# Kernel tuning notes

Measured on AMD Instinct MI355X. Metric: run time of the kernel, lower is better.

Reference implementation:

```python
import jax, jax.numpy as jnp
import numpy as np
import math

B, TSRC, TTGT, DM, DI, H = 2, 2048, 2048, 1024, 1024, 16
DH = DI // H
LN_EPS = 1e-5


def setup_inputs() -> dict:
    key = jax.random.key(0)
    ks = iter(jax.random.split(key, 40))
    def p(*shape):
        return jax.random.normal(next(ks), shape, jnp.float32) * 0.02
    inp = {
        "enc_out_vecs": jax.random.normal(next(ks), (B, TSRC, DM), jnp.float32),
        "output_vecs": jax.random.normal(next(ks), (B, TTGT, DM), jnp.float32),
    }
    for tag in ("dd", "ed"):
        inp["Wq_" + tag] = p(DM, DI); inp["bq_" + tag] = jnp.zeros((DI,), jnp.float32)
        inp["Wk_" + tag] = p(DM, DI); inp["bk_" + tag] = jnp.zeros((DI,), jnp.float32)
        inp["Wv_" + tag] = p(DM, DI); inp["bv_" + tag] = jnp.zeros((DI,), jnp.float32)
        inp["Wo_" + tag] = p(DI, DM); inp["bo_" + tag] = jnp.zeros((DM,), jnp.float32)
        inp["W1_" + tag] = p(DM, 2 * DM); inp["b1_" + tag] = jnp.zeros((2 * DM,), jnp.float32)
        inp["W2_" + tag] = p(2 * DM, DM); inp["b2_" + tag] = jnp.zeros((DM,), jnp.float32)
        inp["g1_" + tag] = jnp.ones((DM,), jnp.float32); inp["be1_" + tag] = jnp.zeros((DM,), jnp.float32)
        inp["g2_" + tag] = jnp.ones((DM,), jnp.float32); inp["be2_" + tag] = jnp.zeros((DM,), jnp.float32)
    return inp


def _ln(x, g, b):
    m = jnp.mean(x, axis=-1, keepdims=True)
    v = jnp.var(x, axis=-1, keepdims=True)
    return (x - m) * jax.lax.rsqrt(v + LN_EPS) * g + b


def _mha(xq, xkv, Wq, bq, Wk, bk, Wv, bv, causal):
    Bb, Tq, _ = xq.shape
    Tk = xkv.shape[1]
    q = (xq @ Wq + bq).reshape(Bb, Tq, H, DH)
    k = (xkv @ Wk + bk).reshape(Bb, Tk, H, DH)
    v = (xkv @ Wv + bv).reshape(Bb, Tk, H, DH)
    s = jnp.einsum("bqhd,bkhd->bhqk", q, k) / math.sqrt(DH)
    if causal:
        mask = jnp.where(jnp.arange(Tk)[None, :] > jnp.arange(Tq)[:, None], -jnp.inf, 0.0)
        s = s + mask
    w = jax.nn.softmax(s, axis=-1)
    return jnp.einsum("bhqk,bkhd->bqhd", w, v).reshape(Bb, Tq, H * DH)


def reference(enc_out_vecs, output_vecs,
              Wq_dd, bq_dd, Wk_dd, bk_dd, Wv_dd, bv_dd, Wo_dd, bo_dd,
              W1_dd, b1_dd, W2_dd, b2_dd, g1_dd, be1_dd, g2_dd, be2_dd,
              Wq_ed, bq_ed, Wk_ed, bk_ed, Wv_ed, bv_ed, Wo_ed, bo_ed,
              W1_ed, b1_ed, W2_ed, b2_ed, g1_ed, be1_ed, g2_ed, be2_ed):
    # masked self-attention over decoder inputs
    x = output_vecs
    a = _mha(x, x, Wq_dd, bq_dd, Wk_dd, bk_dd, Wv_dd, bv_dd, causal=True)
    x = _ln(a @ Wo_dd + bo_dd + x, g1_dd, be1_dd)
    x = _ln(x + jax.nn.relu(x @ W1_dd + b1_dd) @ W2_dd + b2_dd, g2_dd, be2_dd)
    # cross attention against encoder outputs
    a = _mha(x, enc_out_vecs, Wq_ed, bq_ed, Wk_ed, bk_ed, Wv_ed, bv_ed, causal=False)
    x = _ln(a @ Wo_ed + bo_ed + x, g1_ed, be1_ed)
    x = _ln(jax.nn.relu(x @ W1_ed + b1_ed) @ W2_ed + b2_ed + x, g2_ed, be2_ed)
    return x
```

## Files before the change

### kernel.cpp

```cpp
#include <hip/hip_runtime.h>
#include <stdint.h>

#define DEV __device__ __forceinline__
typedef unsigned short u16;
typedef __attribute__((ext_vector_type(8))) short bf16x8;
typedef __attribute__((ext_vector_type(4))) float f32x4;

#define AS1 __attribute__((address_space(1)))
#define AS3 __attribute__((address_space(3)))
#define WAITVM0 asm volatile("s_waitcnt vmcnt(0)" ::: "memory")
#define QSCALE 0.18033688011112042f

DEV u16 f2bf(float f) {
  union { float f; uint32_t u; } x; x.f = f;
  uint32_t r = x.u + 0x7fffu + ((x.u >> 16) & 1u);
  return (u16)(r >> 16);
}

DEV uint32_t cvt_pk_bf16(float a, float b) {
  uint32_t r;
  asm("v_cvt_pk_bf16_f32 %0, %1, %2" : "=v"(r) : "v"(a), "v"(b));
  return r;
}

__global__ __launch_bounds__(256) void k_cvt2(const float* __restrict__ a, const float* __restrict__ bsrc,
                                              u16* __restrict__ oa, u16* __restrict__ ob, int n4) {
  int i = blockIdx.x * blockDim.x + threadIdx.x;
  const float* s;
  u16* o;
  int k;
  if (i < n4) { s = a; o = oa; k = i; }
  else        { s = bsrc; o = ob; k = i - n4; }
  float4 v = reinterpret_cast<const float4*>(s)[k];
  reinterpret_cast<ushort4*>(o)[k] = make_ushort4(f2bf(v.x), f2bf(v.y), f2bf(v.z), f2bf(v.w));
}

struct WTJob { const float* W; u16* WT; int K, M, msh, start; };
struct WTJobs { WTJob j[12]; };

__global__ void k_wT_all(WTJobs jobs) {
  __shared__ float tile[32][33];
  int b = blockIdx.x;
  int i = 0;
#pragma unroll
  for (int t = 1; t < 12; ++t)
    if (b >= jobs.j[t].start) i = t;
  const WTJob J = jobs.j[i];
  int rel = b - J.start;
  int m0 = (rel & ((1 << J.msh) - 1)) << 5;
  int k0 = (rel >> J.msh) << 5;
  int tx = threadIdx.x, ty = threadIdx.y;
#pragma unroll
  for (int q = 0; q < 4; ++q)
    tile[ty + q * 8][tx] = J.W[(size_t)(k0 + ty + q * 8) * J.M + m0 + tx];
  __syncthreads();
#pragma unroll
  for (int q = 0; q < 4; ++q)
    J.WT[(size_t)(m0 + ty + q * 8) * J.K + k0 + tx] = f2bf(tile[tx][ty + q * 8]);
}

template<int R>
DEV void stage_tile(const u16* __restrict__ g, int strideElems, u16* lds, int tid, int wv) {
#pragma unroll
  for (int t = 0; t < R / 32; ++t) {
    int idx = t * 256 + tid;
    int row = idx >> 3;
    int b = (idx & 7) << 4;
    int sb = b ^ ((row & 7) << 4);
    const char* src = (const char*)g + (size_t)row * strideElems * 2 + sb;
    char* dst = (char*)lds + (size_t)(t * 256 + wv * 64) * 16;
    __builtin_amdgcn_global_load_lds((const AS1 void*)src, (AS3 void*)dst, 16, 0, 0);
  }
}

DEV bf16x8 lds_frag(const u16* lds, int row, int kel) {
  int off = row * 128 + ((kel * 2) ^ ((row & 7) << 4));
  return *(const bf16x8*)((const char*)lds + off);
}

template<int JT, int MODE>
__global__ __launch_bounds__(256) void k_gemm(const u16* __restrict__ A, int lda,
                                              const u16* __restrict__ BT,
                                              const float* __restrict__ bias,
                                              void* __restrict__ C, int ldc, int K) {
  constexpr int BN = JT * 32;
  __shared__ __align__(16) u16 A_lds[2][128 * 64];
  __shared__ __align__(16) u16 B_lds[2][BN * 64];
  const int tid = threadIdx.x, lane = tid & 63, wv = tid >> 6;
  const int wm = wv >> 1, wn = wv & 1;
  const int nwg = gridDim.x * gridDim.y;
  const int flat = blockIdx.y * gridDim.x + blockIdx.x;
  const int sw = (flat & 7) * (nwg >> 3) + (flat >> 3);
  const int bx = sw % gridDim.x, by = sw / gridDim.x;
  const int bm0 = by * 128, bn0 = bx * BN;
  const int lr = lane & 15, lk = (lane >> 4) * 8, r0 = (lane >> 4) * 4;

  f32x4 acc[4][JT];
#pragma unroll
  for (int i = 0; i < 4; ++i)
#pragma unroll
    for (int j = 0; j < JT; ++j) acc[i][j] = f32x4{0.f, 0.f, 0.f, 0.f};

  stage_tile<128>(A + (size_t)bm0 * lda, lda, A_lds[0], tid, wv);
  stage_tile<BN>(BT + (size_t)bn0 * K, K, B_lds[0], tid, wv);
  WAITVM0;
  __builtin_amdgcn_s_barrier();

  int cur = 0;
  for (int k0 = 0; k0 < K; k0 += 64) {
    if (k0 + 64 < K) {
      stage_tile<128>(A + (size_t)bm0 * lda + k0 + 64, lda, A_lds[cur ^ 1], tid, wv);
      stage_tile<BN>(BT + (size_t)bn0 * K + k0 + 64, K, B_lds[cur ^ 1], tid, wv);
    }
#pragma unroll
    for (int kk = 0; kk < 2; ++kk) {
      bf16x8 af[4], bfr[JT];
#pragma unroll
      for (int i = 0; i < 4; ++i) af[i] = lds_frag(A_lds[cur], wm * 64 + i * 16 + lr, kk * 32 + lk);
#pragma unroll
      for (int j = 0; j < JT; ++j) bfr[j] = lds_frag(B_lds[cur], wn * (JT * 16) + j * 16 + lr, kk * 32 + lk);
#pragma unroll
      for (int i = 0; i < 4; ++i)
#pragma unroll
        for (int j = 0; j < JT; ++j)
          acc[i][j] = __builtin_amdgcn_mfma_f32_16x16x32_bf16(af[i], bfr[j], acc[i][j], 0, 0, 0);
    }
    WAITVM0;
    __builtin_amdgcn_s_barrier();
    cur ^= 1;
  }

#pragma unroll
  for (int j = 0; j < JT; ++j) {
    int col = bn0 + wn * (JT * 16) + j * 16 + lr;
    float bv = bias[col];
#pragma unroll
    for (int i = 0; i < 4; ++i) {
      int rowb = bm0 + wm * 64 + i * 16 + r0;
      if constexpr (MODE == 0) {
#pragma unroll
        for (int r = 0; r < 4; ++r)
          ((float*)C)[(size_t)(rowb + r) * ldc + col] = acc[i][j][r] + bv;
      } else {
#pragma unroll
        for (int r = 0; r < 4; ++r) {
          float v = fmaxf(acc[i][j][r] + bv, 0.f);
          ((u16*)C)[(size_t)(rowb + r) * ldc + col] = f2bf(v);
        }
      }
    }
  }
}

__global__ __launch_bounds__(256) void k_qkv(const u16* __restrict__ Aq, const u16* __restrict__ Akv,
                                             const u16* __restrict__ BT,
                                             const float* __restrict__ bq, const float* __restrict__ bk,
                                             const float* __restrict__ bv,
                                             u16* __restrict__ Qb, u16* __restrict__ Kb,
                                             u16* __restrict__ Vt, int K) {
  __shared__ __align__(16) u16 A_lds[2][128 * 64];
  __shared__ __align__(16) u16 B_lds[2][128 * 64];
  const int tid = threadIdx.x, lane = tid & 63, wv = tid >> 6;
  const int wm = wv >> 1, wn = wv & 1;
  const int nwg = gridDim.x * gridDim.y;
  const int flat = blockIdx.y * gridDim.x + blockIdx.x;
  const int sw = (flat & 7) * (nwg >> 3) + (flat >> 3);
  const int bx = sw % gridDim.x, by = sw / gridDim.x;
  const int bm0 = by * 128, bn0 = bx * 128;
  const int seg = bn0 >> 10;
  const u16* A = (seg == 0) ? Aq : Akv;
  const int lr = lane & 15, lk = (lane >> 4) * 8, r0 = (lane >> 4) * 4;

  f32x4 acc[4][4];
#pragma unroll
  for (int i = 0; i < 4; ++i)
#pragma unroll
    for (int j = 0; j < 4; ++j) acc[i][j] = f32x4{0.f, 0.f, 0.f, 0.f};

  stage_tile<128>(A + (size_t)bm0 * K, K, A_lds[0], tid, wv);
  stage_tile<128>(BT + (size_t)bn0 * K, K, B_lds[0], tid, wv);
  WAITVM0;
  __builtin_amdgcn_s_barrier();

  int cur = 0;
  for (int k0 = 0; k0 < K; k0 += 64) {
    if (k0 + 64 < K) {
      stage_tile<128>(A + (size_t)bm0 * K + k0 + 64, K, A_lds[cur ^ 1], tid, wv);
      stage_tile<128>(BT + (size_t)bn0 * K + k0 + 64, K, B_lds[cur ^ 1], tid, wv);
    }
#pragma unroll
    for (int kk = 0; kk < 2; ++kk) {
      bf16x8 af[4], bfr[4];
#pragma unroll
      for (int i = 0; i < 4; ++i) af[i] = lds_frag(A_lds[cur], wm * 64 + i * 16 + lr, kk * 32 + lk);
#pragma unroll
      for (int j = 0; j < 4; ++j) bfr[j] = lds_frag(B_lds[cur], wn * 64 + j * 16 + lr, kk * 32 + lk);
#pragma unroll
      for (int i = 0; i < 4; ++i)
#pragma unroll
        for (int j = 0; j < 4; ++j)
          acc[i][j] = __builtin_amdgcn_mfma_f32_16x16x32_bf16(af[i], bfr[j], acc[i][j], 0, 0, 0);
    }
    WAITVM0;
    __builtin_amdgcn_s_barrier();
    cur ^= 1;
  }

#pragma unroll
  for (int j = 0; j < 4; ++j) {
    int col = bn0 + wn * 64 + j * 16 + lr;
    int cl = col & 1023;
#pragma unroll
    for (int i = 0; i < 4; ++i) {
      int rowb = bm0 + wm * 64 + i * 16 + r0;
      if (seg == 0) {
        float bb = bq[cl];
#pragma unroll
        for (int r = 0; r < 4; ++r)
          Qb[(size_t)(rowb + r) * 1024 + cl] = f2bf((acc[i][j][r] + bb) * QSCALE);
      } else if (seg == 1) {
        float bb = bk[cl];
#pragma unroll
        for (int r = 0; r < 4; ++r)
          Kb[(size_t)(rowb + r) * 1024 + cl] = f2bf(acc[i][j][r] + bb);
      } else {
        float bb = bv[cl];
        int bidx = rowb >> 11, t = rowb & 2047;
        ushort4 o = make_ushort4(f2bf(acc[i][j][0] + bb), f2bf(acc[i][j][1] + bb),
                                 f2bf(acc[i][j][2] + bb), f2bf(acc[i][j][3] + bb));
        *reinterpret_cast<ushort4*>(&Vt[((size_t)bidx * 1024 + cl) * 2048 + t]) = o;
      }
    }
  }
}

__global__ __launch_bounds__(256) void k_ln(const float* __restrict__ Rm, const float* __restrict__ X,
                                            const float* __restrict__ g, const float* __restrict__ be,
                                            float* __restrict__ Y, u16* __restrict__ Yb) {
  int row = blockIdx.x;
  size_t base4 = (size_t)row * 256;
  int t = threadIdx.x;
  float4 a = reinterpret_cast<const float4*>(Rm)[base4 + t];
  float4 x = reinterpret_cast<const float4*>(X)[base4 + t];
  float v0 = a.x + x.x, v1 = a.y + x.y, v2 = a.z + x.z, v3 = a.w + x.w;
  float s = v0 + v1 + v2 + v3;
  float ss = v0 * v0 + v1 * v1 + v2 * v2 + v3 * v3;
#pragma unroll
  for (int m = 1; m < 64; m <<= 1) { s += __shfl_xor(s, m); ss += __shfl_xor(ss, m); }
  __shared__ float red[8];
  int wv = t >> 6;
  if ((t & 63) == 0) { red[wv] = s; red[4 + wv] = ss; }
  __syncthreads();
  s = red[0] + red[1] + red[2] + red[3];
  ss = red[4] + red[5] + red[6] + red[7];
  float mean = s * (1.f / 1024.f);
  float var = ss * (1.f / 1024.f) - mean * mean;
  float rstd = rsqrtf(var + 1e-5f);
  float4 gv = reinterpret_cast<const float4*>(g)[t];
  float4 bv = reinterpret_cast<const float4*>(be)[t];
  float o0 = (v0 - mean) * rstd * gv.x + bv.x;
  float o1 = (v1 - mean) * rstd * gv.y + bv.y;
  float o2 = (v2 - mean) * rstd * gv.z + bv.z;
  float o3 = (v3 - mean) * rstd * gv.w + bv.w;
  reinterpret_cast<float4*>(Y)[base4 + t] = make_float4(o0, o1, o2, o3);
  if (Yb) {
    ushort4 ob = make_ushort4(f2bf(o0), f2bf(o1), f2bf(o2), f2bf(o3));
    reinterpret_cast<ushort4*>(Yb)[base4 + t] = ob;
  }
}

template<bool CAUSAL>
__global__ __launch_bounds__(512) void k_attn(const u16* __restrict__ Q, const u16* __restrict__ Kg,
                                              const u16* __restrict__ Vt, u16* __restrict__ O,
                                              float* __restrict__ OP0, float* __restrict__ OP1,
                                              float* __restrict__ L0, float* __restrict__ L1, int T) {
  __shared__ __align__(16) u16 K_lds[3][64 * 64];
  __shared__ __align__(16) u16 V_lds[3][64 * 64];
  __shared__ __align__(16) u16 p_lds[8][16 * 64];
  const int tid = threadIdx.x, lane = tid & 63, wv = tid >> 6;
  const int h = blockIdx.y, b = blockIdx.z;
  const int lq = lane & 15, g = lane >> 4;
  const int swz = (lq & 7) << 4;
  const int fb0 = lq * 128 + ((g * 16) ^ swz);
  const int fb1 = lq * 128 + ((g * 16 + 64) ^ swz);
  const size_t qkbase = ((size_t)b * T) * 1024 + h * 64;
  const size_t vbase = ((size_t)b * 1024 + h * 64) * T;

  int qx, st, en;
  if constexpr (CAUSAL) {
    qx = 15 - (blockIdx.x >> 1);
    const int s = blockIdx.x & 1;
    const int ntf = 2 * qx + 2, half = qx + 1;
    st = s ? half : 0;
    en = s ? ntf : half;
  } else {
    qx = blockIdx.x;
    st = 0;
    en = T >> 6;
  }
  const int qw = qx * 128 + wv * 16;
  const int dtile = qw >> 6;

  bf16x8 aq0, aq1;
  {
    const u16* qp_ = Q + qkbase + (size_t)(qw + lq) * 1024 + g * 8;
    aq0 = *reinterpret_cast<const bf16x8*>(qp_);
    aq1 = *reinterpret_cast<const bf16x8*>(qp_ + 32);
  }

  const int srow = tid >> 3;
  const int ssb = ((tid & 7) << 4) ^ ((srow & 7) << 4);
  const char* ksrc = (const char*)(Kg + qkbase) + (size_t)srow * 2048 + ssb + (size_t)st * 131072;
  const char* vsrc = (const char*)(Vt + vbase) + (size_t)srow * ((size_t)T * 2) + ssb + (size_t)st * 128;
  const uint32_t doff = (uint32_t)(wv << 10);

  auto stage = [&](int buf) {
    __builtin_amdgcn_global_load_lds((const AS1 void*)ksrc, (AS3 void*)((char*)K_lds[buf] + doff), 16, 0, 0);
    __builtin_amdgcn_global_load_lds((const AS1 void*)vsrc, (AS3 void*)((char*)V_lds[buf] + doff), 16, 0, 0);
    ksrc += 131072;
    vsrc += 128;
  };

  f32x4 acc[4];
  float lsum = 0.f;
#pragma unroll
  for (int j = 0; j < 4; ++j) acc[j] = f32x4{0.f, 0.f, 0.f, 0.f};

  char* pw = (char*)p_lds[wv];

  auto qstep = [&](bool domask, int kv0, const char* kb, const char* vb) {
    f32x4 st_[4];
    __builtin_amdgcn_s_setprio(1);
#pragma unroll
    for (int j = 0; j < 4; ++j) {
      bf16x8 bk0 = *reinterpret_cast<const bf16x8*>(kb + fb0 + j * 2048);
      bf16x8 bk1 = *reinterpret_cast<const bf16x8*>(kb + fb1 + j * 2048);
      f32x4 t0 = f32x4{0.f, 0.f, 0.f, 0.f};
      t0 = __builtin_amdgcn_mfma_f32_16x16x32_bf16(bk0, aq0, t0, 0, 0, 0);
      t0 = __builtin_amdgcn_mfma_f32_16x16x32_bf16(bk1, aq1, t0, 0, 0, 0);
      st_[j] = t0;
    }
    __builtin_amdgcn_s_setprio(0);
    uint32_t pk[8];
    if (domask) {
      const int qrow = qw + lq;
#pragma unroll
      for (int j = 0; j < 4; ++j) {
        float p0 = __builtin_exp2f(st_[j][0]);
        float p1 = __builtin_exp2f(st_[j][1]);
        float p2 = __builtin_exp2f(st_[j][2]);
        float p3 = __builtin_exp2f(st_[j][3]);
        int kvb = kv0 + j * 16 + g * 4;
        p0 = (kvb > qrow) ? 0.f : p0;
        p1 = (kvb + 1 > qrow) ? 0.f : p1;
        p2 = (kvb + 2 > qrow) ? 0.f : p2;
        p3 = (kvb + 3 > qrow) ? 0.f : p3;
        lsum += (p0 + p1) + (p2 + p3);
        pk[2 * j] = cvt_pk_bf16(p0, p1);
        pk[2 * j + 1] = cvt_pk_bf16(p2, p3);
      }
    } else {
#pragma unroll
      for (int j = 0; j < 4; ++j) {
        float p0 = __builtin_exp2f(st_[j][0]);
        float p1 = __builtin_exp2f(st_[j][1]);
        float p2 = __builtin_exp2f(st_[j][2]);
        float p3 = __builtin_exp2f(st_[j][3]);
        lsum += (p0 + p1) + (p2 + p3);
        pk[2 * j] = cvt_pk_bf16(p0, p1);
        pk[2 * j + 1] = cvt_pk_bf16(p2, p3);
      }
    }
#pragma unroll
    for (int j = 0; j < 4; ++j)
      *reinterpret_cast<uint2*>(pw + lq * 128 + ((j * 32 + g * 8) ^ swz)) =
          make_uint2(pk[2 * j], pk[2 * j + 1]);
    bf16x8 pf0 = *reinterpret_cast<const bf16x8*>(pw + fb0);
    bf16x8 pf1 = *reinterpret_cast<const bf16x8*>(pw + fb1);
    __builtin_amdgcn_s_setprio(1);
#pragma unroll
    for (int j2 = 0; j2 < 4; ++j2) {
      bf16x8 v0 = *reinterpret_cast<const bf16x8*>(vb + fb0 + j2 * 2048);
      bf16x8 v1 = *reinterpret_cast<const bf16x8*>(vb + fb1 + j2 * 2048);
      acc[j2] = __builtin_amdgcn_mfma_f32_16x16x32_bf16(v0, pf0, acc[j2], 0, 0, 0);
      acc[j2] = __builtin_amdgcn_mfma_f32_16x16x32_bf16(v1, pf1, acc[j2], 0, 0, 0);
    }
    __builtin_amdgcn_s_setprio(0);
  };

  stage(0);
  if (st + 1 < en) {
    stage(1);
    asm volatile("s_waitcnt vmcnt(2)" ::: "memory");
  } else {
    WAITVM0;
  }
  __builtin_amdgcn_s_barrier();

  for (int it = st; it < en; ++it) {
    const int idx = it - st;
    if (it + 2 < en) stage((idx + 2) % 3);
    const char* kb = (const char*)K_lds[idx % 3];
    const char* vb = (const char*)V_lds[idx % 3];
    if (!CAUSAL || it <= dtile)
      qstep(CAUSAL && it == dtile, it << 6, kb, vb);
    if (it + 2 < en) {
      asm volatile("s_waitcnt vmcnt(2)" ::: "memory");
    } else {
      WAITVM0;
    }
    __builtin_amdgcn_s_barrier();
  }

  lsum += __shfl_xor(lsum, 16);
  lsum += __shfl_xor(lsum, 32);
  if constexpr (CAUSAL) {
    float* OP = (blockIdx.x & 1) ? OP1 : OP0;
    float* Lp = (blockIdx.x & 1) ? L1 : L0;
    const int row = (b * 16 + h) * 2048 + qw + lq;
    float* pr = OP + (size_t)row * 64;
#pragma unroll
    for (int j2 = 0; j2 < 4; ++j2)
      *reinterpret_cast<f32x4*>(pr + j2 * 16 + g * 4) = acc[j2];
    if (g == 0) Lp[row] = lsum;
  } else {
    float inv = 1.f / lsum;
    size_t rb = qkbase + (size_t)(qw + lq) * 1024;
#pragma unroll
    for (int j2 = 0; j2 < 4; ++j2) {
      ushort4 o = make_ushort4(f2bf(acc[j2][0] * inv), f2bf(acc[j2][1] * inv),
                               f2bf(acc[j2][2] * inv), f2bf(acc[j2][3] * inv));
      *reinterpret_cast<ushort4*>(&O[rb + j2 * 16 + g * 4]) = o;
    }
  }
}

__global__ __launch_bounds__(256) void k_amrg(const float* __restrict__ P0, const float* __restrict__ P1,
                                              const float* __restrict__ L0, const float* __restrict__ L1,
                                              u16* __restrict__ Ab) {
  int i = blockIdx.x * 256 + threadIdx.x;
  int row = i >> 4, d4 = (i & 15) << 2;
  f32x4 a = *reinterpret_cast<const f32x4*>(&P0[(size_t)row * 64 + d4]);
  f32x4 c = *reinterpret_cast<const f32x4*>(&P1[(size_t)row * 64 + d4]);
  float inv = 1.f / (L0[row] + L1[row]);
  int bh = row >> 11, q = row & 2047, bb = bh >> 4, hh = bh & 15;
  size_t dst = ((size_t)(bb * 2048 + q)) * 1024 + hh * 64 + d4;
  ushort4 o = make_ushort4(f2bf((a[0] + c[0]) * inv), f2bf((a[1] + c[1]) * inv),
                           f2bf((a[2] + c[2]) * inv), f2bf((a[3] + c[3]) * inv));
  *reinterpret_cast<ushort4*>(&Ab[dst]) = o;
}

extern "C" void kernel_launch(void* const* d_in, const int* in_sizes, int n_in,
                              void* d_out, int out_size, void* d_ws, size_t ws_size,
                              hipStream_t stream) {
  const int T = 2048;
  const float* enc = (const float*)d_in[0];
  const float* outv = (const float*)d_in[1];
  auto F = [&](int i) { return (const float*)d_in[i]; };

  size_t off = 0;
  auto alloc = [&](size_t bytes) {
    void* p = (char*)d_ws + off;
    off += (bytes + 255) & ~(size_t)255;
    return p;
  };

  const int tdK[12] = {1024, 1024, 1024, 1024, 1024, 2048, 1024, 1024, 1024, 1024, 1024, 2048};
  const int tdM[12] = {1024, 1024, 1024, 1024, 2048, 1024, 1024, 1024, 1024, 1024, 2048, 1024};
  const int tdIdx[12] = {2, 4, 6, 8, 10, 12, 18, 20, 22, 24, 26, 28};
  u16* WT_[12];
  for (int i = 0; i < 12; ++i) WT_[i] = (u16*)alloc((size_t)tdK[i] * tdM[i] * 2);

  u16* Xb0 = (u16*)alloc(4096ull * 1024 * 2);
  u16* Eb = (u16*)alloc(4096ull * 1024 * 2);
  u16* Qb = (u16*)alloc(4096ull * 1024 * 2);
  u16* Kb = (u16*)alloc(4096ull * 1024 * 2);
  u16* Vt = (u16*)alloc(4096ull * 1024 * 2);
  u16* Ab = (u16*)alloc(4096ull * 1024 * 2);
  u16* Hb = (u16*)alloc(4096ull * 2048 * 2);
  u16* Xbc = (u16*)alloc(4096ull * 1024 * 2);
  float* Rf = (float*)alloc(4096ull * 1024 * 4);
  float* Xfa = (float*)alloc(4096ull * 1024 * 4);
  float* Xfb = (float*)alloc(4096ull * 1024 * 4);
  float* Lsum = (float*)alloc(2ull * 65536 * 4);

  k_cvt2<<<8192, 256, 0, stream>>>(outv, enc, Xb0, Eb, 4096 * 1024 / 4);

  WTJobs jobs;
  int start = 0;
  for (int i = 0; i < 12; ++i) {
    int msh = (tdM[i] == 2048) ? 6 : 5;
    jobs.j[i] = {F(tdIdx[i]), WT_[i], tdK[i], tdM[i], msh, start};
    start += (tdM[i] >> 5) * (tdK[i] >> 5);
  }
  k_wT_all<<<start, dim3(32, 8), 0, stream>>>(jobs);

  float* OP0 = Rf;
  float* OP1 = (float*)Hb;
  float* L0 = Lsum;
  float* L1 = Lsum + 65536;

  dim3 gq(24, 32);
  dim3 g1k(16, 32);
  dim3 g2k(16, 32);
  dim3 gac(32, 16, 2);
  dim3 gan(16, 16, 2);

  k_qkv<<<gq, 256, 0, stream>>>(Xb0, Xb0, WT_[0], F(3), F(5), F(7), Qb, Kb, Vt, 1024);
  k_attn<true><<<gac, 512, 0, stream>>>(Qb, Kb, Vt, Ab, OP0, OP1, L0, L1, T);
  k_amrg<<<4096, 256, 0, stream>>>(OP0, OP1, L0, L1, Ab);
  k_gemm<2, 0><<<g1k, 256, 0, stream>>>(Ab, 1024, WT_[3], F(9), Rf, 1024, 1024);
  k_ln<<<4096, 256, 0, stream>>>(Rf, outv, F(14), F(15), Xfa, Xbc);
  k_gemm<4, 2><<<g2k, 256, 0, stream>>>(Xbc, 1024, WT_[4], F(11), Hb, 2048, 1024);
  k_gemm<2, 0><<<g1k, 256, 0, stream>>>(Hb, 2048, WT_[5], F(13), Rf, 1024, 2048);
  k_ln<<<4096, 256, 0, stream>>>(Rf, Xfa, F(16), F(17), Xfb, Xbc);

  k_qkv<<<gq, 256, 0, stream>>>(Xbc, Eb, WT_[6], F(19), F(21), F(23), Qb, Kb, Vt, 1024);
  k_attn<false><<<gan, 512, 0, stream>>>(Qb, Kb, Vt, Ab, OP0, OP1, L0, L1, T);
  k_gemm<2, 0><<<g1k, 256, 0, stream>>>(Ab, 1024, WT_[9], F(25), Rf, 1024, 1024);
  k_ln<<<4096, 256, 0, stream>>>(Rf, Xfb, F(30), F(31), Xfa, Xbc);
  k_gemm<4, 2><<<g2k, 256, 0, stream>>>(Xbc, 1024, WT_[10], F(27), Hb, 2048, 1024);
  k_gemm<2, 0><<<g1k, 256, 0, stream>>>(Hb, 2048, WT_[11], F(29), Rf, 1024, 2048);
  k_ln<<<4096, 256, 0, stream>>>(Rf, Xfa, F(32), F(33), (float*)d_out, (u16*)nullptr);
}
```

Baseline: 444.6 us.

## Store residual stream, GEMM outputs and attention partials in bf16

The output-projection and FFN2 GEMMs now write bf16 instead of fp32. LayerNorm reads bf16 residual inputs and writes only a bf16 activation, except for the final fp32 output. The causal attention partial outputs are also stored as bf16 in their own buffers. This roughly halves memory traffic in the epilogues, LN kernels and merge kernel, at the cost of extra rounding in the residual path. Residuals now come from bf16 copies rather than fp32, so accuracy drops.

After: 423.3 us. 1.05x faster.

```diff
diff --git a/kernel.cpp b/kernel.cpp
--- a/kernel.cpp
+++ b/kernel.cpp
@@ -15,6 +15,11 @@
   union { float f; uint32_t u; } x; x.f = f;
   uint32_t r = x.u + 0x7fffu + ((x.u >> 16) & 1u);
   return (u16)(r >> 16);
+}
+
+DEV float bf2f(u16 h) {
+  union { uint32_t u; float f; } x; x.u = ((uint32_t)h) << 16;
+  return x.f;
 }
 
 DEV uint32_t cvt_pk_bf16(float a, float b) {
@@ -82,7 +87,7 @@
 __global__ __launch_bounds__(256) void k_gemm(const u16* __restrict__ A, int lda,
                                               const u16* __restrict__ BT,
                                               const float* __restrict__ bias,
-                                              void* __restrict__ C, int ldc, int K) {
+                                              u16* __restrict__ C, int ldc, int K) {
   constexpr int BN = JT * 32;
   __shared__ __align__(16) u16 A_lds[2][128 * 64];
   __shared__ __align__(16) u16 B_lds[2][BN * 64];
@@ -137,16 +142,11 @@
 #pragma unroll
     for (int i = 0; i < 4; ++i) {
       int rowb = bm0 + wm * 64 + i * 16 + r0;
-      if constexpr (MODE == 0) {
-#pragma unroll
-        for (int r = 0; r < 4; ++r)
-          ((float*)C)[(size_t)(rowb + r) * ldc + col] = acc[i][j][r] + bv;
-      } else {
-#pragma unroll
-        for (int r = 0; r < 4; ++r) {
-          float v = fmaxf(acc[i][j][r] + bv, 0.f);
-          ((u16*)C)[(size_t)(rowb + r) * ldc + col] = f2bf(v);
-        }
+#pragma unroll
+      for (int r = 0; r < 4; ++r) {
+        float v = acc[i][j][r] + bv;
+        if constexpr (MODE == 2) v = fmaxf(v, 0.f);
+        C[(size_t)(rowb + r) * ldc + col] = f2bf(v);
       }
     }
   }
@@ -234,15 +234,16 @@
   }
 }
 
-__global__ __launch_bounds__(256) void k_ln(const float* __restrict__ Rm, const float* __restrict__ X,
-                                            const float* __restrict__ g, const float* __restrict__ be,
-                                            float* __restrict__ Y, u16* __restrict__ Yb) {
+__global__ __launch_bounds__(256) void k_ln_b(const u16* __restrict__ Rm, const u16* __restrict__ X,
+                                              const float* __restrict__ g, const float* __restrict__ be,
+                                              u16* __restrict__ Yb, float* __restrict__ Yf) {
   int row = blockIdx.x;
   size_t base4 = (size_t)row * 256;
   int t = threadIdx.x;
-  float4 a = reinterpret_cast<const float4*>(Rm)[base4 + t];
-  float4 x = reinterpret_cast<const float4*>(X)[base4 + t];
-  float v0 = a.x + x.x, v1 = a.y + x.y, v2 = a.z + x.z, v3 = a.w + x.w;
+  ushort4 a4 = reinterpret_cast<const ushort4*>(Rm)[base4 + t];
+  ushort4 x4 = reinterpret_cast<const ushort4*>(X)[base4 + t];
+  float v0 = bf2f(a4.x) + bf2f(x4.x), v1 = bf2f(a4.y) + bf2f(x4.y);
+  float v2 = bf2f(a4.z) + bf2f(x4.z), v3 = bf2f(a4.w) + bf2f(x4.w);
   float s = v0 + v1 + v2 + v3;
   float ss = v0 * v0 + v1 * v1 + v2 * v2 + v3 * v3;
 #pragma unroll
@@ -262,17 +263,18 @@
   float o1 = (v1 - mean) * rstd * gv.y + bv.y;
   float o2 = (v2 - mean) * rstd * gv.z + bv.z;
   float o3 = (v3 - mean) * rstd * gv.w + bv.w;
-  reinterpret_cast<float4*>(Y)[base4 + t] = make_float4(o0, o1, o2, o3);
   if (Yb) {
     ushort4 ob = make_ushort4(f2bf(o0), f2bf(o1), f2bf(o2), f2bf(o3));
     reinterpret_cast<ushort4*>(Yb)[base4 + t] = ob;
   }
+  if (Yf)
+    reinterpret_cast<float4*>(Yf)[base4 + t] = make_float4(o0, o1, o2, o3);
 }
 
 template<bool CAUSAL>
 __global__ __launch_bounds__(512) void k_attn(const u16* __restrict__ Q, const u16* __restrict__ Kg,
                                               const u16* __restrict__ Vt, u16* __restrict__ O,
-                                              float* __restrict__ OP0, float* __restrict__ OP1,
+                                              u16* __restrict__ OP0, u16* __restrict__ OP1,
                                               float* __restrict__ L0, float* __restrict__ L1, int T) {
   __shared__ __align__(16) u16 K_lds[3][64 * 64];
   __shared__ __align__(16) u16 V_lds[3][64 * 64];
@@ -415,13 +417,14 @@
   lsum += __shfl_xor(lsum, 16);
   lsum += __shfl_xor(lsum, 32);
   if constexpr (CAUSAL) {
-    float* OP = (blockIdx.x & 1) ? OP1 : OP0;
+    u16* OP = (blockIdx.x & 1) ? OP1 : OP0;
     float* Lp = (blockIdx.x & 1) ? L1 : L0;
     const int row = (b * 16 + h) * 2048 + qw + lq;
-    float* pr = OP + (size_t)row * 64;
+    u16* pr = OP + (size_t)row * 64;
 #pragma unroll
     for (int j2 = 0; j2 < 4; ++j2)
-      *reinterpret_cast<f32x4*>(pr + j2 * 16 + g * 4) = acc[j2];
+      *reinterpret_cast<uint2*>(pr + j2 * 16 + g * 4) =
+          make_uint2(cvt_pk_bf16(acc[j2][0], acc[j2][1]), cvt_pk_bf16(acc[j2][2], acc[j2][3]));
     if (g == 0) Lp[row] = lsum;
   } else {
     float inv = 1.f / lsum;
@@ -435,18 +438,18 @@
   }
 }
 
-__global__ __launch_bounds__(256) void k_amrg(const float* __restrict__ P0, const float* __restrict__ P1,
+__global__ __launch_bounds__(256) void k_amrg(const u16* __restrict__ P0, const u16* __restrict__ P1,
                                               const float* __restrict__ L0, const float* __restrict__ L1,
                                               u16* __restrict__ Ab) {
   int i = blockIdx.x * 256 + threadIdx.x;
   int row = i >> 4, d4 = (i & 15) << 2;
-  f32x4 a = *reinterpret_cast<const f32x4*>(&P0[(size_t)row * 64 + d4]);
-  f32x4 c = *reinterpret_cast<const f32x4*>(&P1[(size_t)row * 64 + d4]);
+  ushort4 a4 = *reinterpret_cast<const ushort4*>(&P0[(size_t)row * 64 + d4]);
+  ushort4 c4 = *reinterpret_cast<const ushort4*>(&P1[(size_t)row * 64 + d4]);
   float inv = 1.f / (L0[row] + L1[row]);
   int bh = row >> 11, q = row & 2047, bb = bh >> 4, hh = bh & 15;
   size_t dst = ((size_t)(bb * 2048 + q)) * 1024 + hh * 64 + d4;
-  ushort4 o = make_ushort4(f2bf((a[0] + c[0]) * inv), f2bf((a[1] + c[1]) * inv),
-                           f2bf((a[2] + c[2]) * inv), f2bf((a[3] + c[3]) * inv));
+  ushort4 o = make_ushort4(f2bf((bf2f(a4.x) + bf2f(c4.x)) * inv), f2bf((bf2f(a4.y) + bf2f(c4.y)) * inv),
+                           f2bf((bf2f(a4.z) + bf2f(c4.z)) * inv), f2bf((bf2f(a4.w) + bf2f(c4.w)) * inv));
   *reinterpret_cast<ushort4*>(&Ab[dst]) = o;
 }
 
@@ -478,10 +481,12 @@
   u16* Vt = (u16*)alloc(4096ull * 1024 * 2);
   u16* Ab = (u16*)alloc(4096ull * 1024 * 2);
   u16* Hb = (u16*)alloc(4096ull * 2048 * 2);
-  u16* Xbc = (u16*)alloc(4096ull * 1024 * 2);
-  float* Rf = (float*)alloc(4096ull * 1024 * 4);
-  float* Xfa = (float*)alloc(4096ull * 1024 * 4);
-  float* Xfb = (float*)alloc(4096ull * 1024 * 4);
+  u16* Rm = (u16*)alloc(4096ull * 1024 * 2);
+  u16* X1b = (u16*)alloc(4096ull * 1024 * 2);
+  u16* X2b = (u16*)alloc(4096ull * 1024 * 2);
+  u16* X3b = (u16*)alloc(4096ull * 1024 * 2);
+  u16* OP0 = (u16*)alloc(4096ull * 1024 * 2);
+  u16* OP1 = (u16*)alloc(4096ull * 1024 * 2);
   float* Lsum = (float*)alloc(2ull * 65536 * 4);
 
   k_cvt2<<<8192, 256, 0, stream>>>(outv, enc, Xb0, Eb, 4096 * 1024 / 4);
@@ -495,8 +500,6 @@
   }
   k_wT_all<<<start, dim3(32, 8), 0, stream>>>(jobs);
 
-  float* OP0 = Rf;
-  float* OP1 = (float*)Hb;
   float* L0 = Lsum;
   float* L1 = Lsum + 65536;
 
@@ -509,17 +512,17 @@
   k_qkv<<<gq, 256, 0, stream>>>(Xb0, Xb0, WT_[0], F(3), F(5), F(7), Qb, Kb, Vt, 1024);
   k_attn<true><<<gac, 512, 0, stream>>>(Qb, Kb, Vt, Ab, OP0, OP1, L0, L1, T);
   k_amrg<<<4096, 256, 0, stream>>>(OP0, OP1, L0, L1, Ab);
-  k_gemm<2, 0><<<g1k, 256, 0, stream>>>(Ab, 1024, WT_[3], F(9), Rf, 1024, 1024);
-  k_ln<<<4096, 256, 0, stream>>>(Rf, outv, F(14), F(15), Xfa, Xbc);
-  k_gemm<4, 2><<<g2k, 256, 0, stream>>>(Xbc, 1024, WT_[4], F(11), Hb, 2048, 1024);
-  k_gemm<2, 0><<<g1k, 256, 0, stream>>>(Hb, 2048, WT_[5], F(13), Rf, 1024, 2048);
-  k_ln<<<4096, 256, 0, stream>>>(Rf, Xfa, F(16), F(17), Xfb, Xbc);
-
-  k_qkv<<<gq, 256, 0, stream>>>(Xbc, Eb, WT_[6], F(19), F(21), F(23), Qb, Kb, Vt, 1024);
+  k_gemm<2, 1><<<g1k, 256, 0, stream>>>(Ab, 1024, WT_[3], F(9), Rm, 1024, 1024);
+  k_ln_b<<<4096, 256, 0, stream>>>(Rm, Xb0, F(14), F(15), X1b, nullptr);
+  k_gemm<4, 2><<<g2k, 256, 0, stream>>>(X1b, 1024, WT_[4], F(11), Hb, 2048, 1024);
+  k_gemm<2, 1><<<g1k, 256, 0, stream>>>(Hb, 2048, WT_[5], F(13), Rm, 1024, 2048);
+  k_ln_b<<<4096, 256, 0, stream>>>(Rm, X1b, F(16), F(17), X2b, nullptr);
+
+  k_qkv<<<gq, 256, 0, stream>>>(X2b, Eb, WT_[6], F(19), F(21), F(23), Qb, Kb, Vt, 1024);
   k_attn<false><<<gan, 512, 0, stream>>>(Qb, Kb, Vt, Ab, OP0, OP1, L0, L1, T);
-  k_gemm<2, 0><<<g1k, 256, 0, stream>>>(Ab, 1024, WT_[9], F(25), Rf, 1024, 1024);
-  k_ln<<<4096, 256, 0, stream>>>(Rf, Xfb, F(30), F(31), Xfa, Xbc);
-  k_gemm<4, 2><<<g2k, 256, 0, stream>>>(Xbc, 1024, WT_[10], F(27), Hb, 2048, 1024);
-  k_gemm<2, 0><<<g1k, 256, 0, stream>>>(Hb, 2048, WT_[11], F(29), Rf, 1024, 2048);
-  k_ln<<<4096, 256, 0, stream>>>(Rf, Xfa, F(32), F(33), (float*)d_out, (u16*)nullptr);
-}
+  k_gemm<2, 1><<<g1k, 256, 0, stream>>>(Ab, 1024, WT_[9], F(25), Rm, 1024, 1024);
+  k_ln_b<<<4096, 256, 0, stream>>>(Rm, X2b, F(30), F(31), X3b, nullptr);
+  k_gemm<4, 2><<<g2k, 256, 0, stream>>>(X3b, 1024, WT_[10], F(27), Hb, 2048, 1024);
+  k_gemm<2, 1><<<g1k, 256, 0, stream>>>(Hb, 2048, WT_[11], F(29), Rm, 1024, 2048);
+  k_ln_b<<<4096, 256, 0, stream>>>(Rm, X3b, F(32), F(33), nullptr, (float*)d_out);
+}
```
